# Kernel tuning notes

Measured on AMD Instinct MI355X. Metric: run time of the kernel, lower is better.

## Reference

```python
import jax, jax.numpy as jnp
import numpy as np

EPS = 1e-5  # torch LayerNorm default eps

def _layernorm(x):
    mu = x.mean(axis=-1, keepdims=True)
    var = x.var(axis=-1, keepdims=True)  # biased, matches torch
    return (x - mu) / jnp.sqrt(var + EPS)

def setup_inputs() -> dict:
    key = jax.random.key(0)
    k1, k2, k3, k4, k5 = jax.random.split(key, 5)
    B, T, E, H = 8, 2048, 512, 8
    d = E // H
    return {
        "input1": jax.random.normal(k1, (B, T, E), dtype=jnp.float32),
        "Wq": jax.random.normal(k2, (H, d), dtype=jnp.float32) * 0.1,
        "Wk": jax.random.normal(k3, (H, d), dtype=jnp.float32) * 0.1,
        "Wv": jax.random.normal(k4, (H, d, d), dtype=jnp.float32) * 0.1,
        "Wm": jax.random.normal(k5, (E, E), dtype=jnp.float32) * 0.05,
    }

def reference(input1, Wq, Wk, Wv, Wm):
    B, T, E = input1.shape
    H, d = Wq.shape
    xn = _layernorm(input1)                       # norm1 over Embed_Dim
    xh = xn.reshape(B, T, H, d)                   # per-head slices of last dim
    # QLayer surrogates: scalar query/key per token, d-dim value per token
    Q = jnp.einsum('bthd,hd->bht', xh, Wq)        # [B,H,T]
    K = jnp.einsum('bthd,hd->bht', xh, Wk)        # [B,H,T]
    V = jnp.einsum('bthd,hde->bhte', xh, Wv)      # [B,H,T,d]
    # distance attention: A = -(Q_i - K_j)^2
    A = -(Q[:, :, :, None] - K[:, :, None, :]) ** 2   # [B,H,T,T]
    P = jax.nn.softmax(A / (d ** 0.5), axis=-1)
    O = jnp.einsum('bhts,bhse->bhte', P, V)       # [B,H,T,d]
    head_result = O.transpose(0, 2, 1, 3).reshape(B, T, E)  # concat heads
    return head_result @ Wm + input1              # merger + residual
```

## Files before the change

kernel.cpp:

```cpp
#include <hip/hip_runtime.h>

typedef __bf16 bf16x8 __attribute__((ext_vector_type(8)));
typedef short short8 __attribute__((ext_vector_type(8)));
typedef float f32x4 __attribute__((ext_vector_type(4)));

#define TT 2048
#define EE 512
#define NH 8
#define DD 64

#define QSCALE 0.36067376022224085f
#define CSCALE 0.18033688011112042f

__device__ __forceinline__ ushort f2bf(float f) {
  union { float f; unsigned u; } a; a.f = f;
  unsigned u = a.u;
  return (ushort)((u + 0x7FFFu + ((u >> 16) & 1u)) >> 16);
}

__global__ __launch_bounds__(256) void k_ln(
    const float* __restrict__ x, const float* __restrict__ Wq,
    const float* __restrict__ Wk,
    float* __restrict__ Q, float* __restrict__ K, ushort* __restrict__ xnb) {
  const int token = blockIdx.x * 4 + (threadIdx.x >> 6);
  const int l = threadIdx.x & 63;
  const float* xr = x + (size_t)token * EE + l * 8;
  float4 a = *(const float4*)xr;
  float4 c = *(const float4*)(xr + 4);
  float xv[8] = {a.x, a.y, a.z, a.w, c.x, c.y, c.z, c.w};
  float s = 0.f, s2 = 0.f;
#pragma unroll
  for (int i = 0; i < 8; i++) { s += xv[i]; s2 = fmaf(xv[i], xv[i], s2); }
#pragma unroll
  for (int o = 32; o; o >>= 1) { s += __shfl_xor(s, o); s2 += __shfl_xor(s2, o); }
  const float mean = s * (1.f / 512.f);
  const float var = s2 * (1.f / 512.f) - mean * mean;
  const float rstd = rsqrtf(var + 1e-5f);

  float xn[8];
  short8 ob;
#pragma unroll
  for (int i = 0; i < 8; i++) {
    xn[i] = (xv[i] - mean) * rstd;
    ob[i] = (short)f2bf(xn[i]);
  }
  *(short8*)(xnb + (size_t)token * EE + l * 8) = ob;

  const float* wq = Wq + l * 8;
  const float* wk = Wk + l * 8;
  float4 q1 = *(const float4*)wq, q2 = *(const float4*)(wq + 4);
  float4 k1 = *(const float4*)wk, k2 = *(const float4*)(wk + 4);
  float wqv[8] = {q1.x, q1.y, q1.z, q1.w, q2.x, q2.y, q2.z, q2.w};
  float wkv[8] = {k1.x, k1.y, k1.z, k1.w, k2.x, k2.y, k2.z, k2.w};
  float q = 0.f, k = 0.f;
#pragma unroll
  for (int i = 0; i < 8; i++) { q = fmaf(xn[i], wqv[i], q); k = fmaf(xn[i], wkv[i], k); }
#pragma unroll
  for (int o = 4; o; o >>= 1) { q += __shfl_xor(q, o); k += __shfl_xor(k, o); }
  if ((l & 7) == 0) {
    const int h = l >> 3;
    const int b = token >> 11, t = token & (TT - 1);
    const int bh = b * NH + h;
    Q[bh * TT + t] = q * QSCALE;
    K[bh * TT + t] = k;
  }
}

__global__ __launch_bounds__(256) void k_tr(const ushort* __restrict__ xnb,
                                            ushort* __restrict__ xnt) {
  const int bh = blockIdx.y;
  const int b = bh >> 3, h = bh & 7;
  const int t0 = blockIdx.x * 64;
  const int tid = threadIdx.x;
  __shared__ ushort tile[64][72];

  {
    const int i = tid >> 3, ec = (tid & 7) * 8;
    const ushort* src = xnb + (size_t)(b * TT + t0 + i) * EE + h * DD + ec;
    *(uint4*)&tile[i][ec] = *(const uint4*)src;
    *(uint4*)&tile[i + 32][ec] = *(const uint4*)(src + 32 * EE);
  }
  __syncthreads();
  {
    const int e = tid >> 3, chunk = tid & 7, tc = (tid & 7) * 8;
    union { uint4 v; ushort u[8]; } o0, o1;
#pragma unroll
    for (int i = 0; i < 8; i++) {
      o0.u[i] = tile[tc + i][e];
      o1.u[i] = tile[tc + i][e + 32];
    }
    const int soff = ((chunk ^ (e & 7)) << 3);
    ushort* dst = xnt + (size_t)(bh * DD + e) * TT + t0 + soff;
    *(uint4*)dst = o0.v;
    *(uint4*)(dst + (size_t)32 * TT) = o1.v;
  }
}

__global__ __launch_bounds__(256) void k_wvm(
    const float* __restrict__ Wv, const float* __restrict__ Wm,
    ushort* __restrict__ Wvmt) {
  const int k = blockIdx.x;
  const int h = k >> 6;
  const int tid = threadIdx.x;
  __shared__ float wv[64];
  if (tid < 64) wv[tid] = Wv[k * 64 + tid];
  __syncthreads();
  float a0 = 0.f, a1 = 0.f;
#pragma unroll 8
  for (int e = 0; e < 64; e++) {
    const float w = wv[e];
    const float* row = Wm + (size_t)(h * 64 + e) * EE;
    a0 = fmaf(w, row[tid], a0);
    a1 = fmaf(w, row[tid + 256], a1);
  }
  Wvmt[(size_t)tid * EE + k] = f2bf(a0);
  Wvmt[(size_t)(tid + 256) * EE + k] = f2bf(a1);
}

__global__ __launch_bounds__(256, 2) void k_attn(
    const float* __restrict__ Q, const float* __restrict__ K,
    const ushort* __restrict__ xnt, ushort* __restrict__ hr) {
  const int sw = (blockIdx.x & 7) * 64 + (blockIdx.x >> 3);
  const int bh = sw >> 3;
  const int q0 = (sw & 7) * 256;
  const int b = bh >> 3, h = bh & 7;
  const int tid = threadIdx.x;
  const int w = tid >> 6, l = tid & 63;
  const int l16 = l & 15, lhi = l >> 4;

  __shared__ float ks[TT];
  __shared__ float cs[TT];
  __shared__ ushort vt[2][64 * 64];

  {
    const float* Kb = K + bh * TT;
#pragma unroll
    for (int i = 0; i < 8; i++) {
      float kv = Kb[tid + i * 256];
      ks[tid + i * 256] = kv;
      cs[tid + i * 256] = -kv * kv * CSCALE;
    }
  }

  const ushort* Xs = xnt + (size_t)bh * (DD * TT);
  const int se = tid >> 3;
  const int sc = (tid & 7) * 8;
  uint4 st0, st1;

#define ISSUE_STAGE(jt_) do {                                                  \
    st0 = *(const uint4*)(Xs + (size_t)se * TT + (jt_) + sc);                  \
    st1 = *(const uint4*)(Xs + (size_t)(se + 32) * TT + (jt_) + sc);           \
  } while (0)

#define WRITE_STAGE(buf_) do {                                                 \
    *(uint4*)&vt[buf_][se * 64 + sc] = st0;                                    \
    *(uint4*)&vt[buf_][(se + 32) * 64 + sc] = st1;                             \
  } while (0)

  ISSUE_STAGE(0);
  WRITE_STAGE(0);
  __syncthreads();

  float qv[4];
#pragma unroll
  for (int f = 0; f < 4; f++) qv[f] = Q[bh * TT + q0 + w * 64 + f * 16 + l16];

  f32x4 acc[4][4];
  f32x4 accd[4];
#pragma unroll
  for (int f = 0; f < 4; f++) {
    accd[f] = (f32x4){0.f, 0.f, 0.f, 0.f};
#pragma unroll
    for (int c = 0; c < 4; c++) acc[f][c] = (f32x4){0.f, 0.f, 0.f, 0.f};
  }
  short8 onesbits = {0x3F80, 0x3F80, 0x3F80, 0x3F80, 0x3F80, 0x3F80, 0x3F80, 0x3F80};
  const bf16x8 ones = __builtin_bit_cast(bf16x8, onesbits);

  int p = 0;
  for (int jt = 0; jt < TT; jt += 64) {
    const bool more = (jt + 64) < TT;
    if (more) ISSUE_STAGE(jt + 64);

    __builtin_amdgcn_s_setprio(1);
#pragma unroll
    for (int kk = 0; kk < 2; kk++) {
      bf16x8 vf[4];
#pragma unroll
      for (int c = 0; c < 4; c++) {
        const int e = c * 16 + l16;
        vf[c] = *(const bf16x8*)&vt[p][e * 64 + (((kk * 4 + lhi) ^ (e & 7)) << 3)];
      }
      const int jb = jt + kk * 32 + lhi * 8;
      float4 ka = *(const float4*)&ks[jb];
      float4 kb2 = *(const float4*)&ks[jb + 4];
      float4 ca = *(const float4*)&cs[jb];
      float4 cb2 = *(const float4*)&cs[jb + 4];
      float kv8[8] = {ka.x, ka.y, ka.z, ka.w, kb2.x, kb2.y, kb2.z, kb2.w};
      float cv8[8] = {ca.x, ca.y, ca.z, ca.w, cb2.x, cb2.y, cb2.z, cb2.w};
#pragma unroll
      for (int f = 0; f < 4; f++) {
        bf16x8 pa;
#pragma unroll
        for (int i = 0; i < 8; i++)
          pa[i] = (__bf16)__builtin_amdgcn_exp2f(fmaf(qv[f], kv8[i], cv8[i]));
        accd[f] = __builtin_amdgcn_mfma_f32_16x16x32_bf16(pa, ones, accd[f], 0, 0, 0);
#pragma unroll
        for (int c = 0; c < 4; c++)
          acc[f][c] = __builtin_amdgcn_mfma_f32_16x16x32_bf16(pa, vf[c], acc[f][c], 0, 0, 0);
      }
    }
    __builtin_amdgcn_s_setprio(0);

    if (more) WRITE_STAGE(p ^ 1);
    __syncthreads();
    p ^= 1;
  }
#undef ISSUE_STAGE
#undef WRITE_STAGE

#pragma unroll
  for (int f = 0; f < 4; f++) {
#pragma unroll
    for (int r = 0; r < 4; r++) {
      const float rinv = 1.f / accd[f][r];
      const int qrow = q0 + w * 64 + f * 16 + lhi * 4 + r;
      const size_t base = ((size_t)(b * TT + qrow)) * EE + h * DD + l16;
#pragma unroll
      for (int c = 0; c < 4; c++)
        hr[base + c * 16] = f2bf(acc[f][c][r] * rinv);
    }
  }
}

__global__ __launch_bounds__(256, 2) void k_merge(
    const ushort* __restrict__ hr, const ushort* __restrict__ Wmt,
    const float* __restrict__ x, float* __restrict__ out) {
  const int n0 = blockIdx.x * 128;
  const int m0 = blockIdx.y * 128;
  const int tid = threadIdx.x;
  const int w = tid >> 6, l = tid & 63;
  const int l16 = l & 15, lhi = l >> 4;
  const int wm = w >> 1, wn = w & 1;

  __shared__ ushort As[2][128 * 72];
  __shared__ ushort Bs[2][128 * 72];
  f32x4 acc[4][4];
#pragma unroll
  for (int i = 0; i < 4; i++)
#pragma unroll
    for (int j = 0; j < 4; j++) acc[i][j] = (f32x4){0.f, 0.f, 0.f, 0.f};

  const int row = tid >> 1, half = tid & 1;
  const ushort* sa0 = hr + (size_t)(m0 + row) * EE + half * 32;
  const ushort* sb0 = Wmt + (size_t)(n0 + row) * EE + half * 32;

  {
    uint4* da = (uint4*)&As[0][row * 72 + half * 32];
    uint4* db = (uint4*)&Bs[0][row * 72 + half * 32];
#pragma unroll
    for (int i = 0; i < 4; i++) da[i] = *(const uint4*)(sa0 + i * 8);
#pragma unroll
    for (int i = 0; i < 4; i++) db[i] = *(const uint4*)(sb0 + i * 8);
  }
  __syncthreads();

  int p = 0;
  for (int k0 = 0; k0 < EE; k0 += 64) {
    const bool more = (k0 + 64) < EE;
    uint4 pa[4], pb[4];
    if (more) {
#pragma unroll
      for (int i = 0; i < 4; i++) pa[i] = *(const uint4*)(sa0 + k0 + 64 + i * 8);
#pragma unroll
      for (int i = 0; i < 4; i++) pb[i] = *(const uint4*)(sb0 + k0 + 64 + i * 8);
    }
#pragma unroll
    for (int kk = 0; kk < 2; kk++) {
      bf16x8 af[4], bfr[4];
#pragma unroll
      for (int mi = 0; mi < 4; mi++)
        af[mi] = *(const bf16x8*)&As[p][(wm * 64 + mi * 16 + l16) * 72 + kk * 32 + lhi * 8];
#pragma unroll
      for (int ni = 0; ni < 4; ni++)
        bfr[ni] = *(const bf16x8*)&Bs[p][(wn * 64 + ni * 16 + l16) * 72 + kk * 32 + lhi * 8];
#pragma unroll
      for (int mi = 0; mi < 4; mi++)
#pragma unroll
        for (int ni = 0; ni < 4; ni++)
          acc[mi][ni] = __builtin_amdgcn_mfma_f32_16x16x32_bf16(af[mi], bfr[ni], acc[mi][ni], 0, 0, 0);
    }
    if (more) {
      uint4* da = (uint4*)&As[p ^ 1][row * 72 + half * 32];
      uint4* db = (uint4*)&Bs[p ^ 1][row * 72 + half * 32];
#pragma unroll
      for (int i = 0; i < 4; i++) da[i] = pa[i];
#pragma unroll
      for (int i = 0; i < 4; i++) db[i] = pb[i];
    }
    __syncthreads();
    p ^= 1;
  }

#pragma unroll
  for (int mi = 0; mi < 4; mi++) {
#pragma unroll
    for (int r = 0; r < 4; r++) {
      const int grow = m0 + wm * 64 + mi * 16 + lhi * 4 + r;
#pragma unroll
      for (int ni = 0; ni < 4; ni++) {
        const int gcol = n0 + wn * 64 + ni * 16 + l16;
        size_t idx = (size_t)grow * EE + gcol;
        out[idx] = acc[mi][ni][r] + x[idx];
      }
    }
  }
}

extern "C" void kernel_launch(void* const* d_in, const int* in_sizes, int n_in,
                              void* d_out, int out_size, void* d_ws, size_t ws_size,
                              hipStream_t stream) {
  const float* x  = (const float*)d_in[0];
  const float* Wq = (const float*)d_in[1];
  const float* Wk = (const float*)d_in[2];
  const float* Wv = (const float*)d_in[3];
  const float* Wm = (const float*)d_in[4];
  float* out = (float*)d_out;

  char* ws = (char*)d_ws;
  float*  Qp   = (float*)(ws);
  float*  Kp   = (float*)(ws + 524288);
  ushort* xnb  = (ushort*)(ws + 1048576);
  ushort* hrp  = (ushort*)(ws + 1048576);
  ushort* xnt  = (ushort*)(ws + 17825792);
  ushort* Wvmt = (ushort*)(ws + 34603008);

  k_ln<<<4096, 256, 0, stream>>>(x, Wq, Wk, Qp, Kp, xnb);
  k_tr<<<dim3(TT / 64, 8 * NH), 256, 0, stream>>>(xnb, xnt);
  k_wvm<<<EE, 256, 0, stream>>>(Wv, Wm, Wvmt);
  k_attn<<<512, 256, 0, stream>>>(Qp, Kp, xnt, hrp);
  k_merge<<<dim3(EE / 128, (8 * TT) / 128), 256, 0, stream>>>(hrp, Wvmt, x, out);
}
```

Before: 123.9 us.

## Deepen attention V staging to 256-key chunks, recompute K^2 term, swizzle and vectorize merge

The attention kernel now stages four 64-key V tiles per pipeline step, with two register batches whose global loads and LDS writes are interleaved between tile computations. This cuts the number of block barriers and hides more load latency, at the cost of more LDS (64KB for vt) and registers. The per-key -k^2 constant is now recomputed in registers instead of being kept in a separate LDS array. The merge GEMM remaps block indices so that neighbouring tiles land on the same XCD, and its epilogue goes through LDS so the residual add and output store use coalesced float4 accesses.

```diff
diff --git a/kernel.cpp b/kernel.cpp
--- a/kernel.cpp
+++ b/kernel.cpp
@@ -129,36 +129,35 @@
   const int l16 = l & 15, lhi = l >> 4;
 
   __shared__ float ks[TT];
-  __shared__ float cs[TT];
-  __shared__ ushort vt[2][64 * 64];
+  __shared__ ushort vt[2][4][64 * 64];
 
   {
     const float* Kb = K + bh * TT;
 #pragma unroll
-    for (int i = 0; i < 8; i++) {
-      float kv = Kb[tid + i * 256];
-      ks[tid + i * 256] = kv;
-      cs[tid + i * 256] = -kv * kv * CSCALE;
-    }
+    for (int i = 0; i < 8; i++) ks[tid + i * 256] = Kb[tid + i * 256];
   }
 
   const ushort* Xs = xnt + (size_t)bh * (DD * TT);
   const int se = tid >> 3;
   const int sc = (tid & 7) * 8;
-  uint4 st0, st1;
-
-#define ISSUE_STAGE(jt_) do {                                                  \
-    st0 = *(const uint4*)(Xs + (size_t)se * TT + (jt_) + sc);                  \
-    st1 = *(const uint4*)(Xs + (size_t)(se + 32) * TT + (jt_) + sc);           \
+  uint4 stA[4], stB[4];
+
+#define ISSUE(st, jp_) do {                                                    \
+    st[0] = *(const uint4*)(Xs + (size_t)se * TT + (jp_) + sc);                \
+    st[1] = *(const uint4*)(Xs + (size_t)(se + 32) * TT + (jp_) + sc);         \
+    st[2] = *(const uint4*)(Xs + (size_t)se * TT + (jp_) + 64 + sc);           \
+    st[3] = *(const uint4*)(Xs + (size_t)(se + 32) * TT + (jp_) + 64 + sc);    \
   } while (0)
 
-#define WRITE_STAGE(buf_) do {                                                 \
-    *(uint4*)&vt[buf_][se * 64 + sc] = st0;                                    \
-    *(uint4*)&vt[buf_][(se + 32) * 64 + sc] = st1;                             \
+#define WRITEST(st, buf_, t0_) do {                                            \
+    *(uint4*)&vt[buf_][t0_][se * 64 + sc] = st[0];                             \
+    *(uint4*)&vt[buf_][t0_][(se + 32) * 64 + sc] = st[1];                      \
+    *(uint4*)&vt[buf_][(t0_) + 1][se * 64 + sc] = st[2];                       \
+    *(uint4*)&vt[buf_][(t0_) + 1][(se + 32) * 64 + sc] = st[3];                \
   } while (0)
 
-  ISSUE_STAGE(0);
-  WRITE_STAGE(0);
+  ISSUE(stA, 0);   WRITEST(stA, 0, 0);
+  ISSUE(stB, 128); WRITEST(stB, 0, 2);
   __syncthreads();
 
   float qv[4];
@@ -176,47 +175,58 @@
   short8 onesbits = {0x3F80, 0x3F80, 0x3F80, 0x3F80, 0x3F80, 0x3F80, 0x3F80, 0x3F80};
   const bf16x8 ones = __builtin_bit_cast(bf16x8, onesbits);
 
-  int p = 0;
-  for (int jt = 0; jt < TT; jt += 64) {
-    const bool more = (jt + 64) < TT;
-    if (more) ISSUE_STAGE(jt + 64);
-
+#define TILE(cur_, tt_, jt_) do {                                              \
+    _Pragma("unroll") for (int kk = 0; kk < 2; kk++) {                         \
+      bf16x8 vf[4];                                                            \
+      _Pragma("unroll") for (int c = 0; c < 4; c++) {                          \
+        const int e = c * 16 + l16;                                            \
+        vf[c] = *(const bf16x8*)&vt[cur_][tt_][e * 64 +                        \
+                    (((kk * 4 + lhi) ^ (e & 7)) << 3)];                        \
+      }                                                                        \
+      const int jb = (jt_) + kk * 32 + lhi * 8;                                \
+      float4 ka = *(const float4*)&ks[jb];                                     \
+      float4 kb2 = *(const float4*)&ks[jb + 4];                                \
+      float kv8[8] = {ka.x, ka.y, ka.z, ka.w, kb2.x, kb2.y, kb2.z, kb2.w};     \
+      float cv8[8];                                                            \
+      _Pragma("unroll") for (int i = 0; i < 8; i++) {                          \
+        float m = kv8[i] * (-CSCALE);                                          \
+        cv8[i] = m * kv8[i];                                                   \
+      }                                                                        \
+      _Pragma("unroll") for (int f = 0; f < 4; f++) {                          \
+        bf16x8 pa;                                                             \
+        _Pragma("unroll") for (int i = 0; i < 8; i++)                          \
+          pa[i] = (__bf16)__builtin_amdgcn_exp2f(fmaf(qv[f], kv8[i], cv8[i])); \
+        accd[f] = __builtin_amdgcn_mfma_f32_16x16x32_bf16(pa, ones, accd[f], 0, 0, 0); \
+        _Pragma("unroll") for (int c = 0; c < 4; c++)                          \
+          acc[f][c] = __builtin_amdgcn_mfma_f32_16x16x32_bf16(pa, vf[c], acc[f][c], 0, 0, 0); \
+      }                                                                        \
+    }                                                                          \
+  } while (0)
+
+  int cur = 0;
+  for (int pp = 0; pp < 8; pp++) {
+    const int jp = pp * 256;
+    const bool more = pp < 7;
+    if (more) ISSUE(stA, jp + 256);
     __builtin_amdgcn_s_setprio(1);
-#pragma unroll
-    for (int kk = 0; kk < 2; kk++) {
-      bf16x8 vf[4];
-#pragma unroll
-      for (int c = 0; c < 4; c++) {
-        const int e = c * 16 + l16;
-        vf[c] = *(const bf16x8*)&vt[p][e * 64 + (((kk * 4 + lhi) ^ (e & 7)) << 3)];
-      }
-      const int jb = jt + kk * 32 + lhi * 8;
-      float4 ka = *(const float4*)&ks[jb];
-      float4 kb2 = *(const float4*)&ks[jb + 4];
-      float4 ca = *(const float4*)&cs[jb];
-      float4 cb2 = *(const float4*)&cs[jb + 4];
-      float kv8[8] = {ka.x, ka.y, ka.z, ka.w, kb2.x, kb2.y, kb2.z, kb2.w};
-      float cv8[8] = {ca.x, ca.y, ca.z, ca.w, cb2.x, cb2.y, cb2.z, cb2.w};
-#pragma unroll
-      for (int f = 0; f < 4; f++) {
-        bf16x8 pa;
-#pragma unroll
-        for (int i = 0; i < 8; i++)
-          pa[i] = (__bf16)__builtin_amdgcn_exp2f(fmaf(qv[f], kv8[i], cv8[i]));
-        accd[f] = __builtin_amdgcn_mfma_f32_16x16x32_bf16(pa, ones, accd[f], 0, 0, 0);
-#pragma unroll
-        for (int c = 0; c < 4; c++)
-          acc[f][c] = __builtin_amdgcn_mfma_f32_16x16x32_bf16(pa, vf[c], acc[f][c], 0, 0, 0);
-      }
-    }
+    TILE(cur, 0, jp);
+    TILE(cur, 1, jp + 64);
     __builtin_amdgcn_s_setprio(0);
-
-    if (more) WRITE_STAGE(p ^ 1);
+    if (more) {
+      WRITEST(stA, cur ^ 1, 0);
+      ISSUE(stB, jp + 256 + 128);
+    }
+    __builtin_amdgcn_s_setprio(1);
+    TILE(cur, 2, jp + 128);
+    TILE(cur, 3, jp + 192);
+    __builtin_amdgcn_s_setprio(0);
+    if (more) WRITEST(stB, cur ^ 1, 2);
     __syncthreads();
-    p ^= 1;
-  }
-#undef ISSUE_STAGE
-#undef WRITE_STAGE
+    cur ^= 1;
+  }
+#undef ISSUE
+#undef WRITEST
+#undef TILE
 
 #pragma unroll
   for (int f = 0; f < 4; f++) {
@@ -235,15 +245,19 @@
 __global__ __launch_bounds__(256, 2) void k_merge(
     const ushort* __restrict__ hr, const ushort* __restrict__ Wmt,
     const float* __restrict__ x, float* __restrict__ out) {
-  const int n0 = blockIdx.x * 128;
-  const int m0 = blockIdx.y * 128;
+  const int fid = blockIdx.y * 4 + blockIdx.x;
+  const int xcd = fid & 7, idx = fid >> 3;
+  const int n0 = (idx & 3) * 128;
+  const int m0 = (xcd * 16 + (idx >> 2)) * 128;
   const int tid = threadIdx.x;
   const int w = tid >> 6, l = tid & 63;
   const int l16 = l & 15, lhi = l >> 4;
   const int wm = w >> 1, wn = w & 1;
 
-  __shared__ ushort As[2][128 * 72];
-  __shared__ ushort Bs[2][128 * 72];
+  __shared__ ushort smem[36864];
+#define AS(p) (smem + (p) * 9216)
+#define BS(p) (smem + 18432 + (p) * 9216)
+
   f32x4 acc[4][4];
 #pragma unroll
   for (int i = 0; i < 4; i++)
@@ -255,8 +269,8 @@
   const ushort* sb0 = Wmt + (size_t)(n0 + row) * EE + half * 32;
 
   {
-    uint4* da = (uint4*)&As[0][row * 72 + half * 32];
-    uint4* db = (uint4*)&Bs[0][row * 72 + half * 32];
+    uint4* da = (uint4*)&AS(0)[row * 72 + half * 32];
+    uint4* db = (uint4*)&BS(0)[row * 72 + half * 32];
 #pragma unroll
     for (int i = 0; i < 4; i++) da[i] = *(const uint4*)(sa0 + i * 8);
 #pragma unroll
@@ -279,10 +293,10 @@
       bf16x8 af[4], bfr[4];
 #pragma unroll
       for (int mi = 0; mi < 4; mi++)
-        af[mi] = *(const bf16x8*)&As[p][(wm * 64 + mi * 16 + l16) * 72 + kk * 32 + lhi * 8];
+        af[mi] = *(const bf16x8*)&AS(p)[(wm * 64 + mi * 16 + l16) * 72 + kk * 32 + lhi * 8];
 #pragma unroll
       for (int ni = 0; ni < 4; ni++)
-        bfr[ni] = *(const bf16x8*)&Bs[p][(wn * 64 + ni * 16 + l16) * 72 + kk * 32 + lhi * 8];
+        bfr[ni] = *(const bf16x8*)&BS(p)[(wn * 64 + ni * 16 + l16) * 72 + kk * 32 + lhi * 8];
 #pragma unroll
       for (int mi = 0; mi < 4; mi++)
 #pragma unroll
@@ -290,8 +304,8 @@
           acc[mi][ni] = __builtin_amdgcn_mfma_f32_16x16x32_bf16(af[mi], bfr[ni], acc[mi][ni], 0, 0, 0);
     }
     if (more) {
-      uint4* da = (uint4*)&As[p ^ 1][row * 72 + half * 32];
-      uint4* db = (uint4*)&Bs[p ^ 1][row * 72 + half * 32];
+      uint4* da = (uint4*)&AS(p ^ 1)[row * 72 + half * 32];
+      uint4* db = (uint4*)&BS(p ^ 1)[row * 72 + half * 32];
 #pragma unroll
       for (int i = 0; i < 4; i++) da[i] = pa[i];
 #pragma unroll
@@ -301,19 +315,34 @@
     p ^= 1;
   }
 
+  float* ldsf = (float*)smem;
 #pragma unroll
   for (int mi = 0; mi < 4; mi++) {
 #pragma unroll
     for (int r = 0; r < 4; r++) {
-      const int grow = m0 + wm * 64 + mi * 16 + lhi * 4 + r;
-#pragma unroll
-      for (int ni = 0; ni < 4; ni++) {
-        const int gcol = n0 + wn * 64 + ni * 16 + l16;
-        size_t idx = (size_t)grow * EE + gcol;
-        out[idx] = acc[mi][ni][r] + x[idx];
-      }
-    }
-  }
+      const int orow = wm * 64 + mi * 16 + lhi * 4 + r;
+#pragma unroll
+      for (int ni = 0; ni < 4; ni++)
+        ldsf[orow * 132 + wn * 64 + ni * 16 + l16] = acc[mi][ni][r];
+    }
+  }
+  __syncthreads();
+  {
+    const int orow = tid >> 1, cb = (tid & 1) * 64;
+    const int grow = m0 + orow;
+    const float* xr = x + (size_t)grow * EE + n0 + cb;
+    float* og = out + (size_t)grow * EE + n0 + cb;
+    const float* lr = ldsf + orow * 132 + cb;
+#pragma unroll
+    for (int i = 0; i < 16; i++) {
+      float4 xa = *(const float4*)(xr + i * 4);
+      float4 v = *(const float4*)(lr + i * 4);
+      v.x += xa.x; v.y += xa.y; v.z += xa.z; v.w += xa.w;
+      *(float4*)(og + i * 4) = v;
+    }
+  }
+#undef AS
+#undef BS
 }
 
 extern "C" void kernel_launch(void* const* d_in, const int* in_sizes, int n_in,
```

Result: slower. 142.3 us (+14.8%).
